# Kernel optimization log

Measured on AMD Instinct MI355X. Metric: run time of the kernel, lower is better.

The kernel has to match this reference:

```python
import jax, jax.numpy as jnp
import numpy as np
from jax import lax

B, Ht, Wt, C, NH, KV, FF = 32, 32, 32, 768, 12, 16, 4
HD = C // NH
EPS = 1e-5


def setup_inputs() -> dict:
    key = jax.random.key(0)
    ks = jax.random.split(key, 12)
    rn = lambda k, s, sc=0.02: jax.random.normal(k, s, jnp.float32) * sc
    inp = {"x": jax.random.normal(ks[0], (B, Ht * Wt, C), jnp.float32)}
    inp["ln1_g"] = jnp.ones((C,), jnp.float32)
    inp["ln1_b"] = jnp.zeros((C,), jnp.float32)
    for i, nm in enumerate(["q", "k", "v"]):
        inp[f"dw_w_{nm}"] = rn(ks[1 + i], (C, 1, 3, 3), 0.1)
        inp[f"dw_b_{nm}"] = jnp.zeros((C,), jnp.float32)
        inp[f"bn_g_{nm}"] = jnp.ones((C,), jnp.float32)
        inp[f"bn_b_{nm}"] = jnp.zeros((C,), jnp.float32)
        inp[f"bn_m_{nm}"] = jnp.zeros((C,), jnp.float32)
        inp[f"bn_v_{nm}"] = jnp.ones((C,), jnp.float32)
        inp[f"W_{nm}"] = rn(ks[4 + i], (C, C))
        inp[f"b_{nm}"] = jnp.zeros((C,), jnp.float32)
    inp["ln2_g"] = jnp.ones((C,), jnp.float32)
    inp["ln2_b"] = jnp.zeros((C,), jnp.float32)
    inp["W1"] = rn(ks[7], (FF * C, C))
    inp["b1"] = jnp.zeros((FF * C,), jnp.float32)
    inp["W2"] = rn(ks[8], (C, FF * C))
    inp["b2"] = jnp.zeros((C,), jnp.float32)
    return inp


def _ln(x, g, b):
    m = jnp.mean(x, -1, keepdims=True)
    v = jnp.var(x, -1, keepdims=True)
    return (x - m) * lax.rsqrt(v + EPS) * g + b


def _dw_branch(x4, w, bias, g, bb, m, v, stride):
    # depthwise conv (groups=C) -> ELU -> BatchNorm (eval) -> b (h w) c
    y = lax.conv_general_dilated(
        x4, w, (stride, stride), [(1, 1), (1, 1)],
        feature_group_count=C,
        dimension_numbers=("NCHW", "OIHW", "NCHW"),
    ) + bias[None, :, None, None]
    y = jax.nn.elu(y)
    y = (y - m[None, :, None, None]) * lax.rsqrt(v + EPS)[None, :, None, None] \
        * g[None, :, None, None] + bb[None, :, None, None]
    return y.reshape(B, C, -1).transpose(0, 2, 1)  # (B, n, C)


def _heads(t, Wm, bm):
    t = t @ Wm.T + bm                         # (B, n, C)
    n = t.shape[1]
    return t.reshape(B, n, NH, HD).transpose(0, 2, 1, 3)  # (B, H, n, d)


def reference(x, ln1_g, ln1_b,
              dw_w_q, dw_b_q, bn_g_q, bn_b_q, bn_m_q, bn_v_q, W_q, b_q,
              dw_w_k, dw_b_k, bn_g_k, bn_b_k, bn_m_k, bn_v_k, W_k, b_k,
              dw_w_v, dw_b_v, bn_g_v, bn_b_v, bn_m_v, bn_v_v, W_v, b_v,
              ln2_g, ln2_b, W1, b1, W2, b2):
    xn = _ln(x, ln1_g, ln1_b)
    x4 = xn.transpose(0, 2, 1).reshape(B, C, Ht, Wt)
    q = _heads(_dw_branch(x4, dw_w_q, dw_b_q, bn_g_q, bn_b_q, bn_m_q, bn_v_q, 1), W_q, b_q)
    k = _heads(_dw_branch(x4, dw_w_k, dw_b_k, bn_g_k, bn_b_k, bn_m_k, bn_v_k, 2), W_k, b_k)
    v = _heads(_dw_branch(x4, dw_w_v, dw_b_v, bn_g_v, bn_b_v, bn_m_v, bn_v_v, 2), W_v, b_v)
    scale = 1.0 / (HD ** 0.5)
    attn = jnp.einsum("bhnd,bhmd->bhnm", q, k) * scale
    attn = jax.nn.softmax(attn, axis=-1)
    o = jnp.einsum("bhnm,bhmd->bhnd", attn, v)
    o = o.transpose(0, 2, 1, 3).reshape(B, Ht * Wt, C)
    x = x + o  # DropPath is identity at inference
    h = _ln(x, ln2_g, ln2_b)
    h = jax.nn.gelu(h @ W1.T + b1, approximate=False) @ W2.T + b2
    return x + h
```

## Files before the change

### kernel.cpp

```cpp
#include <hip/hip_runtime.h>
#include <math.h>

#define NB   32
#define C_   768
#define NQ   1024
#define NKV  256
#define NH_  12
#define HD_  64
#define FFC  3072
#define EPS_ 1e-5f

typedef __attribute__((ext_vector_type(8))) _Float16 f16x8;
typedef __attribute__((ext_vector_type(4))) _Float16 f16x4;
typedef __attribute__((ext_vector_type(4))) float    f32x4;

__device__ __forceinline__ void gload_lds16(const void* g, void* l) {
  __builtin_amdgcn_global_load_lds((const __attribute__((address_space(1))) void*)g,
                                   (__attribute__((address_space(3))) void*)l, 16, 0, 0);
}

__global__ __launch_bounds__(256)
void ln_fwd_kernel(const float* __restrict__ x, const float* __restrict__ g,
                   const float* __restrict__ b, _Float16* __restrict__ out) {
  const int row = blockIdx.x;
  const float* xr = x + (size_t)row * C_;
  const int t = threadIdx.x;
  float v0 = xr[t], v1 = xr[t + 256], v2 = xr[t + 512];
  float s = v0 + v1 + v2;
  float q = v0 * v0 + v1 * v1 + v2 * v2;
#pragma unroll
  for (int m = 1; m < 64; m <<= 1) { s += __shfl_xor(s, m); q += __shfl_xor(q, m); }
  __shared__ float ls[4], lq[4];
  const int w = t >> 6, lane = t & 63;
  if (lane == 0) { ls[w] = s; lq[w] = q; }
  __syncthreads();
  s = ls[0] + ls[1] + ls[2] + ls[3];
  q = lq[0] + lq[1] + lq[2] + lq[3];
  const float mean = s * (1.f / C_);
  const float rstd = rsqrtf(q * (1.f / C_) - mean * mean + EPS_);
  _Float16* orow = out + (size_t)row * C_;
  orow[t]       = (_Float16)((v0 - mean) * rstd * g[t]       + b[t]);
  orow[t + 256] = (_Float16)((v1 - mean) * rstd * g[t + 256] + b[t + 256]);
  orow[t + 512] = (_Float16)((v2 - mean) * rstd * g[t + 512] + b[t + 512]);
}

__global__ __launch_bounds__(256)
void resln2_kernel(const float* __restrict__ x, const _Float16* __restrict__ o,
                   const float* __restrict__ g, const float* __restrict__ bb,
                   float* __restrict__ xr_out, _Float16* __restrict__ h) {
  const int row = blockIdx.x;
  const float* xp = x + (size_t)row * C_;
  const _Float16* op = o + (size_t)row * C_;
  const int t = threadIdx.x;
  float v[3]; float s = 0.f, q = 0.f;
#pragma unroll
  for (int i = 0; i < 3; i++) {
    int c = t + i * 256;
    v[i] = xp[c] + (float)op[c];
    s += v[i]; q += v[i] * v[i];
  }
#pragma unroll
  for (int m = 1; m < 64; m <<= 1) { s += __shfl_xor(s, m); q += __shfl_xor(q, m); }
  __shared__ float ls[4], lq[4];
  const int w = t >> 6, lane = t & 63;
  if (lane == 0) { ls[w] = s; lq[w] = q; }
  __syncthreads();
  s = ls[0] + ls[1] + ls[2] + ls[3];
  q = lq[0] + lq[1] + lq[2] + lq[3];
  const float mean = s * (1.f / C_);
  const float rstd = rsqrtf(q * (1.f / C_) - mean * mean + EPS_);
#pragma unroll
  for (int i = 0; i < 3; i++) {
    int c = t + i * 256;
    xr_out[(size_t)row * C_ + c] = v[i];
    h[(size_t)row * C_ + c] = (_Float16)((v[i] - mean) * rstd * g[c] + bb[c]);
  }
}

#define SZ_CC (C_ * C_)
#define SZ_CF (FFC * C_)
__global__ void cast_all_kernel(const float* __restrict__ Wq, const float* __restrict__ Wk,
                                const float* __restrict__ Wv, const float* __restrict__ W1,
                                const float* __restrict__ W2,
                                _Float16* __restrict__ oq, _Float16* __restrict__ ok,
                                _Float16* __restrict__ ov, _Float16* __restrict__ o1,
                                _Float16* __restrict__ o2) {
  const int total = 3 * SZ_CC + 2 * SZ_CF;
  int i = blockIdx.x * 256 + threadIdx.x;
  int stride = gridDim.x * 256;
  for (; i < total; i += stride) {
    if (i < SZ_CC)                     oq[i] = (_Float16)Wq[i];
    else if (i < 2 * SZ_CC)            ok[i - SZ_CC] = (_Float16)Wk[i - SZ_CC];
    else if (i < 3 * SZ_CC)            ov[i - 2 * SZ_CC] = (_Float16)Wv[i - 2 * SZ_CC];
    else if (i < 3 * SZ_CC + SZ_CF)    o1[i - 3 * SZ_CC] = (_Float16)W1[i - 3 * SZ_CC];
    else                               o2[i - 3 * SZ_CC - SZ_CF] = (_Float16)W2[i - 3 * SZ_CC - SZ_CF];
  }
}

__global__ __launch_bounds__(256)
void vtrans_kernel(const _Float16* __restrict__ vbuf, _Float16* __restrict__ vT) {
  const int b = blockIdx.z;
  const int c = blockIdx.y * 256 + threadIdx.x;
  const int kvb = blockIdx.x * 64;
#pragma unroll
  for (int kk = 0; kk < 8; kk++) {
    int kv0 = kvb + kk * 8;
    f16x8 v;
#pragma unroll
    for (int j = 0; j < 8; j++)
      v[j] = vbuf[(size_t)((b << 8) + kv0 + j) * C_ + c];
    *(f16x8*)(vT + ((size_t)(b * C_ + c) << 8) + kv0) = v;
  }
}

struct DwP { const float *w, *bias, *g, *b, *m, *v; };

__device__ __forceinline__ float elu_f(float x) {
  return x > 0.f ? x : __expf(x) - 1.f;
}

__global__ __launch_bounds__(256)
void dw_fused_kernel(const _Float16* __restrict__ xn, DwP pq, DwP pk, DwP pv,
                     _Float16* __restrict__ oq, _Float16* __restrict__ ok,
                     _Float16* __restrict__ ov) {
  const int i = blockIdx.x;
  const int b = blockIdx.z;
  const int c = blockIdx.y * 256 + threadIdx.x;
  const _Float16* xb = xn + (size_t)b * NQ * C_ + c;

  float wq[9], wk[9], wv[9];
#pragma unroll
  for (int u = 0; u < 9; u++) {
    wq[u] = pq.w[c * 9 + u]; wk[u] = pk.w[c * 9 + u]; wv[u] = pv.w[c * 9 + u];
  }
  const float skq = rsqrtf(pq.v[c] + EPS_) * pq.g[c], bnq = pq.b[c] - pq.m[c] * skq;
  const float skk = rsqrtf(pk.v[c] + EPS_) * pk.g[c], bnk = pk.b[c] - pk.m[c] * skk;
  const float skv = rsqrtf(pv.v[c] + EPS_) * pv.g[c], bnv = pv.b[c] - pv.m[c] * skv;
  const float cbq = pq.bias[c], cbk = pk.bias[c], cbv = pv.bias[c];

  float t[5][5];
  auto ldc = [&](int s, int iw) {
    const bool cv = (iw >= 0 && iw < 32);
#pragma unroll
    for (int u = 0; u < 5; u++) {
      int ih = 2 * i - 1 + u;
      t[u][s] = (cv && ih >= 0 && ih < 32) ? (float)xb[(size_t)(ih * 32 + iw) * C_] : 0.f;
    }
  };

#pragma unroll
  for (int j = 0; j < 16; j++) {
    if (j == 0) {
      ldc(0, -1); ldc(1, 0); ldc(2, 1); ldc(3, 2); ldc(4, 3);
    } else {
#pragma unroll
      for (int u = 0; u < 5; u++) { t[u][0] = t[u][2]; t[u][1] = t[u][3]; t[u][2] = t[u][4]; }
      ldc(3, 2 * j + 2); ldc(4, 2 * j + 3);
    }
    float ak = cbk, av = cbv;
#pragma unroll
    for (int u = 0; u < 3; u++)
#pragma unroll
      for (int vv = 0; vv < 3; vv++) {
        ak += t[u][vv] * wk[u * 3 + vv];
        av += t[u][vv] * wv[u * 3 + vv];
      }
    ak = elu_f(ak) * skk + bnk;
    av = elu_f(av) * skv + bnv;
    ok[((size_t)b * NKV + i * 16 + j) * C_ + c] = (_Float16)ak;
    ov[((size_t)b * NKV + i * 16 + j) * C_ + c] = (_Float16)av;
#pragma unroll
    for (int a = 0; a < 2; a++)
#pragma unroll
      for (int b2 = 0; b2 < 2; b2++) {
        float aq = cbq;
#pragma unroll
        for (int u = 0; u < 3; u++)
#pragma unroll
          for (int vv = 0; vv < 3; vv++)
            aq += t[a + u][b2 + vv] * wq[u * 3 + vv];
        aq = elu_f(aq) * skq + bnq;
        oq[((size_t)b * NQ + (2 * i + a) * 32 + (2 * j + b2)) * C_ + c] = (_Float16)aq;
      }
  }
}

__device__ __forceinline__ void stage_tile(const _Float16* __restrict__ src, int ldk,
                                           int row0, int kt, _Float16* lds, int w, int lane) {
#pragma unroll
  for (int it = 0; it < 4; it++) {
    int cid = (it * 4 + w) * 64 + lane;
    int row = cid >> 3, kg = cid & 7;
    int kgs = kg ^ (row & 7);
    const _Float16* g = src + (size_t)(row0 + row) * ldk + kt * 64 + kgs * 8;
    gload_lds16((const void*)g, (void*)((char*)lds + (it * 4 + w) * 1024));
  }
}

template <int EPI>
__global__ __launch_bounds__(256, 2)
void gemm_f16(const _Float16* __restrict__ A, const _Float16* __restrict__ Bw,
              const float* __restrict__ bias,
              _Float16* __restrict__ outh, float* __restrict__ outf,
              int M, int N, int K) {
  __shared__ __align__(16) _Float16 lds[2][2][128 * 64];
  const int tid = threadIdx.x, w = tid >> 6, lane = tid & 63;
  const int wm = w >> 1, wn = w & 1;
  const int m0 = blockIdx.x * 128, n0 = blockIdx.y * 128;

  f32x4 acc[4][4];
#pragma unroll
  for (int i = 0; i < 4; i++)
#pragma unroll
    for (int j = 0; j < 4; j++)
#pragma unroll
      for (int r = 0; r < 4; r++) acc[i][j][r] = 0.f;

  stage_tile(A, K, m0, 0, lds[0][0], w, lane);
  stage_tile(Bw, K, n0, 0, lds[0][1], w, lane);
  __syncthreads();
  const int NKT = K >> 6;
  int buf = 0;
  for (int kt = 0; kt < NKT; kt++) {
    if (kt + 1 < NKT) {
      stage_tile(A, K, m0, kt + 1, lds[buf ^ 1][0], w, lane);
      stage_tile(Bw, K, n0, kt + 1, lds[buf ^ 1][1], w, lane);
    }
    f16x8 af[4][2], bfr[4][2];
#pragma unroll
    for (int mi = 0; mi < 4; mi++)
#pragma unroll
      for (int kh = 0; kh < 2; kh++) {
        int row = wm * 64 + mi * 16 + (lane & 15);
        int kg = kh * 4 + (lane >> 4);
        af[mi][kh] = *(const f16x8*)&lds[buf][0][row * 64 + ((kg ^ (row & 7)) << 3)];
      }
#pragma unroll
    for (int ni = 0; ni < 4; ni++)
#pragma unroll
      for (int kh = 0; kh < 2; kh++) {
        int row = wn * 64 + ni * 16 + (lane & 15);
        int kg = kh * 4 + (lane >> 4);
        bfr[ni][kh] = *(const f16x8*)&lds[buf][1][row * 64 + ((kg ^ (row & 7)) << 3)];
      }
#pragma unroll
    for (int mi = 0; mi < 4; mi++)
#pragma unroll
      for (int ni = 0; ni < 4; ni++)
#pragma unroll
        for (int kh = 0; kh < 2; kh++)
          acc[mi][ni] = __builtin_amdgcn_mfma_f32_16x16x32_f16(af[mi][kh], bfr[ni][kh],
                                                               acc[mi][ni], 0, 0, 0);
    __syncthreads();
    buf ^= 1;
  }
#pragma unroll
  for (int mi = 0; mi < 4; mi++)
#pragma unroll
    for (int ni = 0; ni < 4; ni++) {
      int col = n0 + wn * 64 + ni * 16 + (lane & 15);
      float bv = bias[col];
#pragma unroll
      for (int r = 0; r < 4; r++) {
        int rowg = m0 + wm * 64 + mi * 16 + (lane >> 4) * 4 + r;
        float val = acc[mi][ni][r] + bv;
        size_t idx = (size_t)rowg * N + col;
        if (EPI == 0) {
          outh[idx] = (_Float16)val;
        } else if (EPI == 1) {
          float ge = 0.5f * val * (1.f + erff(val * 0.70710678118f));
          outh[idx] = (_Float16)ge;
        } else {
          outf[idx] += val;
        }
      }
    }
}

__global__ __launch_bounds__(512, 2)
void attn_kernel(const _Float16* __restrict__ Q, const _Float16* __restrict__ Kb,
                 const _Float16* __restrict__ vT, _Float16* __restrict__ O) {
  __shared__ __align__(16) _Float16 Klds[256 * 64];
  __shared__ __align__(16) _Float16 Vt[64 * 256];
  const int tid = threadIdx.x, w = tid >> 6, lane = tid & 63;
  const int hi = lane >> 4, lo = lane & 15;
  const int half = blockIdx.x & 1;
  const int h = (blockIdx.x >> 1) % NH_;
  const int b = blockIdx.x / (2 * NH_);

  const _Float16* qp = Q + (size_t)b * NQ * C_ + h * HD_;
  const _Float16* kp = Kb + (size_t)b * NKV * C_ + h * HD_;
  const _Float16* vp = vT + ((size_t)(b * C_ + h * HD_) << 8);

#pragma unroll
  for (int i = 0; i < 4; i++) {
    int cid = i * 512 + w * 64 + lane;
    int row = cid >> 3, kg = cid & 7;
    const _Float16* g = kp + (size_t)row * C_ + ((kg ^ (row & 7)) << 3);
    gload_lds16((const void*)g, (void*)((char*)Klds + (i * 512 + w * 64) * 16));
  }
#pragma unroll
  for (int i = 0; i < 4; i++) {
    int cid = i * 512 + w * 64 + lane;
    int row = cid >> 5, kg = cid & 31;
    const _Float16* g = vp + ((size_t)row << 8) + ((kg ^ (row & 7)) << 3);
    gload_lds16((const void*)g, (void*)((char*)Vt + (i * 512 + w * 64) * 16));
  }
  __syncthreads();

#pragma unroll
  for (int ti = 0; ti < 4; ti++) {
    const int q0 = half * 512 + w * 64 + ti * 16;
    f16x8 qf[2];
#pragma unroll
    for (int kh = 0; kh < 2; kh++)
      qf[kh] = *(const f16x8*)(qp + (size_t)(q0 + lo) * C_ + kh * 32 + hi * 8);
    f32x4 S[16];
#pragma unroll
    for (int nt = 0; nt < 16; nt++) {
      f32x4 s; s[0] = 0.f; s[1] = 0.f; s[2] = 0.f; s[3] = 0.f;
      const _Float16* krow = &Klds[(nt * 16 + lo) * 64];
#pragma unroll
      for (int kh = 0; kh < 2; kh++) {
        f16x8 kf = *(const f16x8*)&krow[((kh * 4 + hi) ^ (lo & 7)) << 3];
        s = __builtin_amdgcn_mfma_f32_16x16x32_f16(kf, qf[kh], s, 0, 0, 0);
      }
      S[nt] = s;
    }
    float mx = -1e30f;
#pragma unroll
    for (int nt = 0; nt < 16; nt++)
#pragma unroll
      for (int r = 0; r < 4; r++) { S[nt][r] *= 0.125f; mx = fmaxf(mx, S[nt][r]); }
    mx = fmaxf(mx, __shfl_xor(mx, 16));
    mx = fmaxf(mx, __shfl_xor(mx, 32));
    float sum = 0.f;
#pragma unroll
    for (int nt = 0; nt < 16; nt++)
#pragma unroll
      for (int r = 0; r < 4; r++) { float e = __expf(S[nt][r] - mx); S[nt][r] = e; sum += e; }
    sum += __shfl_xor(sum, 16);
    sum += __shfl_xor(sum, 32);
    const float inv = 1.f / sum;
    f16x8 pa8[8];
#pragma unroll
    for (int ntp = 0; ntp < 8; ntp++)
#pragma unroll
      for (int r = 0; r < 4; r++) {
        pa8[ntp][r]     = (_Float16)(S[2 * ntp][r] * inv);
        pa8[ntp][4 + r] = (_Float16)(S[2 * ntp + 1][r] * inv);
      }
    f32x4 acc[4];
#pragma unroll
    for (int dt = 0; dt < 4; dt++) { acc[dt][0] = 0.f; acc[dt][1] = 0.f; acc[dt][2] = 0.f; acc[dt][3] = 0.f; }
#pragma unroll
    for (int dt = 0; dt < 4; dt++) {
      const int d = dt * 16 + lo, sw = d & 7;
      const _Float16* vrow = &Vt[d * 256 + 4 * (hi & 1)];
#pragma unroll
      for (int ntp = 0; ntp < 8; ntp++) {
        f16x4 v0 = *(const f16x4*)&vrow[((4 * ntp + (hi >> 1)) ^ sw) << 3];
        f16x4 v1 = *(const f16x4*)&vrow[((4 * ntp + 2 + (hi >> 1)) ^ sw) << 3];
        f16x8 vt8;
#pragma unroll
        for (int r = 0; r < 4; r++) { vt8[r] = v0[r]; vt8[4 + r] = v1[r]; }
        acc[dt] = __builtin_amdgcn_mfma_f32_16x16x32_f16(pa8[ntp], vt8, acc[dt], 0, 0, 0);
      }
    }
#pragma unroll
    for (int dt = 0; dt < 4; dt++)
#pragma unroll
      for (int r = 0; r < 4; r++)
        O[(size_t)(b * NQ + q0 + 4 * hi + r) * C_ + h * HD_ + dt * 16 + lo] = (_Float16)acc[dt][r];
  }
}

extern "C" void kernel_launch(void* const* d_in, const int* in_sizes, int n_in,
                              void* d_out, int out_size, void* d_ws, size_t ws_size,
                              hipStream_t stream) {
  (void)in_sizes; (void)n_in; (void)out_size; (void)ws_size;
  const float* x    = (const float*)d_in[0];
  const float* ln1g = (const float*)d_in[1];
  const float* ln1b = (const float*)d_in[2];
  DwP pq { (const float*)d_in[3], (const float*)d_in[4], (const float*)d_in[5],
           (const float*)d_in[6], (const float*)d_in[7], (const float*)d_in[8] };
  const float* Wq = (const float*)d_in[9];  const float* bq = (const float*)d_in[10];
  DwP pk { (const float*)d_in[11], (const float*)d_in[12], (const float*)d_in[13],
           (const float*)d_in[14], (const float*)d_in[15], (const float*)d_in[16] };
  const float* Wk = (const float*)d_in[17]; const float* bk = (const float*)d_in[18];
  DwP pv { (const float*)d_in[19], (const float*)d_in[20], (const float*)d_in[21],
           (const float*)d_in[22], (const float*)d_in[23], (const float*)d_in[24] };
  const float* Wv = (const float*)d_in[25]; const float* bv = (const float*)d_in[26];
  const float* ln2g = (const float*)d_in[27];
  const float* ln2b = (const float*)d_in[28];
  const float* W1 = (const float*)d_in[29]; const float* b1 = (const float*)d_in[30];
  const float* W2 = (const float*)d_in[31]; const float* b2 = (const float*)d_in[32];

  char* ws = (char*)d_ws;
  _Float16* xn   = (_Float16*)(ws + 0);
  _Float16* o    = xn;
  _Float16* tq   = (_Float16*)(ws + 100663296);
  _Float16* tk   = (_Float16*)(ws + 150994944);
  _Float16* tv   = (_Float16*)(ws + 163577856);
  _Float16* hb   = tq;
  _Float16* vTb  = tv;
  _Float16* qb   = (_Float16*)(ws + 176160768);
  _Float16* gbuf = qb;
  _Float16* kb   = (_Float16*)(ws + 226492416);
  _Float16* vbuf = (_Float16*)(ws + 239075328);
  _Float16* wqh  = (_Float16*)(ws + 251658240);
  _Float16* wkh  = (_Float16*)(ws + 252837888);
  _Float16* wvh  = (_Float16*)(ws + 254017536);
  _Float16* w1h  = (_Float16*)(ws + 255197184);
  _Float16* w2h  = (_Float16*)(ws + 259915776);
  float* out = (float*)d_out;

  ln_fwd_kernel<<<NB * NQ, 256, 0, stream>>>(x, ln1g, ln1b, xn);
  cast_all_kernel<<<2048, 256, 0, stream>>>(Wq, Wk, Wv, W1, W2, wqh, wkh, wvh, w1h, w2h);
  dw_fused_kernel<<<dim3(16, 3, NB), 256, 0, stream>>>(xn, pq, pk, pv, tq, tk, tv);
  gemm_f16<0><<<dim3(256, 6), 256, 0, stream>>>(tq, wqh, bq, qb, nullptr, NB * NQ, C_, C_);
  gemm_f16<0><<<dim3(64, 6), 256, 0, stream>>>(tk, wkh, bk, kb, nullptr, NB * NKV, C_, C_);
  gemm_f16<0><<<dim3(64, 6), 256, 0, stream>>>(tv, wvh, bv, vbuf, nullptr, NB * NKV, C_, C_);
  vtrans_kernel<<<dim3(4, 3, NB), 256, 0, stream>>>(vbuf, vTb);
  attn_kernel<<<NB * NH_ * 2, 512, 0, stream>>>(qb, kb, vTb, o);
  resln2_kernel<<<NB * NQ, 256, 0, stream>>>(x, o, ln2g, ln2b, out, hb);
  for (int mc = 0; mc < 4; mc++) {
    gemm_f16<1><<<dim3(64, 24), 256, 0, stream>>>(hb + (size_t)mc * 8192 * C_, w1h, b1,
                                                  gbuf, nullptr, 8192, FFC, C_);
    gemm_f16<2><<<dim3(64, 6), 256, 0, stream>>>(gbuf, w2h, b2, nullptr,
                                                 out + (size_t)mc * 8192 * C_, 8192, C_, FFC);
  }
}
```

Baseline: 930.6 us.

## Add 256x256-tile GELU GEMM for FFN1, vectorize depthwise conv over channel pairs

Adds a new 512-thread GEMM kernel with 256x256 tiles and a GELU epilogue for the first FFN projection. It uses s_setprio around the MFMA bursts and splits each k-tile into four phases. The FFN now runs in two M-chunks of 16384 rows instead of four chunks of 8192, with the GELU buffer moved to the start of the workspace. The depthwise conv kernel now has each thread handle two adjacent channels with f16x2 loads and stores, using a single 384-thread block per row across all 768 channels. The aim is more data reuse per LDS load in the dominant FFN GEMM and fewer memory transactions in the conv. The cost is higher register and LDS pressure (128 KB LDS per block), which may reduce occupancy.

```diff
diff --git a/kernel.cpp b/kernel.cpp
--- a/kernel.cpp
+++ b/kernel.cpp
@@ -12,6 +12,7 @@
 
 typedef __attribute__((ext_vector_type(8))) _Float16 f16x8;
 typedef __attribute__((ext_vector_type(4))) _Float16 f16x4;
+typedef __attribute__((ext_vector_type(2))) _Float16 f16x2;
 typedef __attribute__((ext_vector_type(4))) float    f32x4;
 
 __device__ __forceinline__ void gload_lds16(const void* g, void* l) {
@@ -119,32 +120,42 @@
   return x > 0.f ? x : __expf(x) - 1.f;
 }
 
-__global__ __launch_bounds__(256)
+__global__ __launch_bounds__(384)
 void dw_fused_kernel(const _Float16* __restrict__ xn, DwP pq, DwP pk, DwP pv,
                      _Float16* __restrict__ oq, _Float16* __restrict__ ok,
                      _Float16* __restrict__ ov) {
   const int i = blockIdx.x;
   const int b = blockIdx.z;
-  const int c = blockIdx.y * 256 + threadIdx.x;
-  const _Float16* xb = xn + (size_t)b * NQ * C_ + c;
-
-  float wq[9], wk[9], wv[9];
+  const int c0 = 2 * threadIdx.x;
+  const _Float16* xb = xn + (size_t)b * NQ * C_ + c0;
+
+  float wqx[9], wqy[9], wkx[9], wky[9], wvx[9], wvy[9];
 #pragma unroll
   for (int u = 0; u < 9; u++) {
-    wq[u] = pq.w[c * 9 + u]; wk[u] = pk.w[c * 9 + u]; wv[u] = pv.w[c * 9 + u];
-  }
-  const float skq = rsqrtf(pq.v[c] + EPS_) * pq.g[c], bnq = pq.b[c] - pq.m[c] * skq;
-  const float skk = rsqrtf(pk.v[c] + EPS_) * pk.g[c], bnk = pk.b[c] - pk.m[c] * skk;
-  const float skv = rsqrtf(pv.v[c] + EPS_) * pv.g[c], bnv = pv.b[c] - pv.m[c] * skv;
-  const float cbq = pq.bias[c], cbk = pk.bias[c], cbv = pv.bias[c];
-
-  float t[5][5];
+    wqx[u] = pq.w[c0 * 9 + u]; wqy[u] = pq.w[(c0 + 1) * 9 + u];
+    wkx[u] = pk.w[c0 * 9 + u]; wky[u] = pk.w[(c0 + 1) * 9 + u];
+    wvx[u] = pv.w[c0 * 9 + u]; wvy[u] = pv.w[(c0 + 1) * 9 + u];
+  }
+  const float skqx = rsqrtf(pq.v[c0] + EPS_) * pq.g[c0], bnqx = pq.b[c0] - pq.m[c0] * skqx;
+  const float skqy = rsqrtf(pq.v[c0+1] + EPS_) * pq.g[c0+1], bnqy = pq.b[c0+1] - pq.m[c0+1] * skqy;
+  const float skkx = rsqrtf(pk.v[c0] + EPS_) * pk.g[c0], bnkx = pk.b[c0] - pk.m[c0] * skkx;
+  const float skky = rsqrtf(pk.v[c0+1] + EPS_) * pk.g[c0+1], bnky = pk.b[c0+1] - pk.m[c0+1] * skky;
+  const float skvx = rsqrtf(pv.v[c0] + EPS_) * pv.g[c0], bnvx = pv.b[c0] - pv.m[c0] * skvx;
+  const float skvy = rsqrtf(pv.v[c0+1] + EPS_) * pv.g[c0+1], bnvy = pv.b[c0+1] - pv.m[c0+1] * skvy;
+  const float cbqx = pq.bias[c0], cbqy = pq.bias[c0+1];
+  const float cbkx = pk.bias[c0], cbky = pk.bias[c0+1];
+  const float cbvx = pv.bias[c0], cbvy = pv.bias[c0+1];
+
+  float tx[5][5], ty[5][5];
   auto ldc = [&](int s, int iw) {
     const bool cv = (iw >= 0 && iw < 32);
 #pragma unroll
     for (int u = 0; u < 5; u++) {
       int ih = 2 * i - 1 + u;
-      t[u][s] = (cv && ih >= 0 && ih < 32) ? (float)xb[(size_t)(ih * 32 + iw) * C_] : 0.f;
+      if (cv && ih >= 0 && ih < 32) {
+        f16x2 p = *(const f16x2*)&xb[(size_t)(ih * 32 + iw) * C_];
+        tx[u][s] = (float)p[0]; ty[u][s] = (float)p[1];
+      } else { tx[u][s] = 0.f; ty[u][s] = 0.f; }
     }
   };
 
@@ -154,33 +165,43 @@
       ldc(0, -1); ldc(1, 0); ldc(2, 1); ldc(3, 2); ldc(4, 3);
     } else {
 #pragma unroll
-      for (int u = 0; u < 5; u++) { t[u][0] = t[u][2]; t[u][1] = t[u][3]; t[u][2] = t[u][4]; }
+      for (int u = 0; u < 5; u++) {
+        tx[u][0] = tx[u][2]; tx[u][1] = tx[u][3]; tx[u][2] = tx[u][4];
+        ty[u][0] = ty[u][2]; ty[u][1] = ty[u][3]; ty[u][2] = ty[u][4];
+      }
       ldc(3, 2 * j + 2); ldc(4, 2 * j + 3);
     }
-    float ak = cbk, av = cbv;
+    float akx = cbkx, aky = cbky, avx = cbvx, avy = cbvy;
 #pragma unroll
     for (int u = 0; u < 3; u++)
 #pragma unroll
       for (int vv = 0; vv < 3; vv++) {
-        ak += t[u][vv] * wk[u * 3 + vv];
-        av += t[u][vv] * wv[u * 3 + vv];
-      }
-    ak = elu_f(ak) * skk + bnk;
-    av = elu_f(av) * skv + bnv;
-    ok[((size_t)b * NKV + i * 16 + j) * C_ + c] = (_Float16)ak;
-    ov[((size_t)b * NKV + i * 16 + j) * C_ + c] = (_Float16)av;
+        akx += tx[u][vv] * wkx[u * 3 + vv]; aky += ty[u][vv] * wky[u * 3 + vv];
+        avx += tx[u][vv] * wvx[u * 3 + vv]; avy += ty[u][vv] * wvy[u * 3 + vv];
+      }
+    f16x2 kv2, vv2;
+    kv2[0] = (_Float16)(elu_f(akx) * skkx + bnkx);
+    kv2[1] = (_Float16)(elu_f(aky) * skky + bnky);
+    vv2[0] = (_Float16)(elu_f(avx) * skvx + bnvx);
+    vv2[1] = (_Float16)(elu_f(avy) * skvy + bnvy);
+    *(f16x2*)&ok[((size_t)b * NKV + i * 16 + j) * C_ + c0] = kv2;
+    *(f16x2*)&ov[((size_t)b * NKV + i * 16 + j) * C_ + c0] = vv2;
 #pragma unroll
     for (int a = 0; a < 2; a++)
 #pragma unroll
       for (int b2 = 0; b2 < 2; b2++) {
-        float aq = cbq;
+        float aqx = cbqx, aqy = cbqy;
 #pragma unroll
         for (int u = 0; u < 3; u++)
 #pragma unroll
-          for (int vv = 0; vv < 3; vv++)
-            aq += t[a + u][b2 + vv] * wq[u * 3 + vv];
-        aq = elu_f(aq) * skq + bnq;
-        oq[((size_t)b * NQ + (2 * i + a) * 32 + (2 * j + b2)) * C_ + c] = (_Float16)aq;
+          for (int vv = 0; vv < 3; vv++) {
+            aqx += tx[a + u][b2 + vv] * wqx[u * 3 + vv];
+            aqy += ty[a + u][b2 + vv] * wqy[u * 3 + vv];
+          }
+        f16x2 q2;
+        q2[0] = (_Float16)(elu_f(aqx) * skqx + bnqx);
+        q2[1] = (_Float16)(elu_f(aqy) * skqy + bnqy);
+        *(f16x2*)&oq[((size_t)b * NQ + (2 * i + a) * 32 + (2 * j + b2)) * C_ + c0] = q2;
       }
   }
 }
@@ -265,14 +286,98 @@
         int rowg = m0 + wm * 64 + mi * 16 + (lane >> 4) * 4 + r;
         float val = acc[mi][ni][r] + bv;
         size_t idx = (size_t)rowg * N + col;
-        if (EPI == 0) {
-          outh[idx] = (_Float16)val;
-        } else if (EPI == 1) {
-          float ge = 0.5f * val * (1.f + erff(val * 0.70710678118f));
-          outh[idx] = (_Float16)ge;
-        } else {
-          outf[idx] += val;
+        if (EPI == 0) outh[idx] = (_Float16)val;
+        else          outf[idx] += val;
+      }
+    }
+}
+
+__global__ __launch_bounds__(512, 2)
+void gemm256_gelu(const _Float16* __restrict__ A, const _Float16* __restrict__ Bw,
+                  const float* __restrict__ bias, _Float16* __restrict__ outh,
+                  int M, int N, int K) {
+  __shared__ __align__(16) _Float16 As[2][256 * 64];
+  __shared__ __align__(16) _Float16 Bs[2][256 * 64];
+  const int tid = threadIdx.x, w = tid >> 6, lane = tid & 63;
+  const int wm = w >> 2, wn = w & 3;
+  const int hi = lane >> 4, lo = lane & 15;
+  const int m0 = blockIdx.x * 256, n0 = blockIdx.y * 256;
+
+  f32x4 acc[8][4];
+#pragma unroll
+  for (int i = 0; i < 8; i++)
+#pragma unroll
+    for (int j = 0; j < 4; j++)
+#pragma unroll
+      for (int r = 0; r < 4; r++) acc[i][j][r] = 0.f;
+
+  auto stage = [&](const _Float16* src, int row0, int kt, _Float16* lds) {
+#pragma unroll
+    for (int it = 0; it < 4; it++) {
+      int cid = it * 512 + tid;
+      int row = cid >> 3, kg = cid & 7;
+      const _Float16* g = src + (size_t)(row0 + row) * K + kt * 64 + ((kg ^ (row & 7)) << 3);
+      gload_lds16((const void*)g, (void*)((char*)lds + (size_t)(it * 512 + w * 64) * 16));
+    }
+  };
+
+  stage(A, m0, 0, As[0]);
+  stage(Bw, n0, 0, Bs[0]);
+  __syncthreads();
+  const int NKT = K >> 6;
+  int buf = 0;
+  for (int kt = 0; kt < NKT; kt++) {
+    if (kt + 1 < NKT) {
+      stage(A, m0, kt + 1, As[buf ^ 1]);
+      stage(Bw, n0, kt + 1, Bs[buf ^ 1]);
+    }
+#pragma unroll
+    for (int ph = 0; ph < 4; ph++) {
+      const int mh = ph & 1, nh = ph >> 1;
+      f16x8 af[4][2], bf[2][2];
+#pragma unroll
+      for (int mi = 0; mi < 4; mi++)
+#pragma unroll
+        for (int kh = 0; kh < 2; kh++) {
+          int row = wm * 128 + mh * 64 + mi * 16 + lo;
+          int kg = kh * 4 + hi;
+          af[mi][kh] = *(const f16x8*)&As[buf][row * 64 + ((kg ^ (row & 7)) << 3)];
         }
+#pragma unroll
+      for (int ni = 0; ni < 2; ni++)
+#pragma unroll
+        for (int kh = 0; kh < 2; kh++) {
+          int row = wn * 64 + nh * 32 + ni * 16 + lo;
+          int kg = kh * 4 + hi;
+          bf[ni][kh] = *(const f16x8*)&Bs[buf][row * 64 + ((kg ^ (row & 7)) << 3)];
+        }
+      __builtin_amdgcn_s_setprio(1);
+#pragma unroll
+      for (int mi = 0; mi < 4; mi++)
+#pragma unroll
+        for (int ni = 0; ni < 2; ni++)
+#pragma unroll
+          for (int kh = 0; kh < 2; kh++)
+            acc[mh * 4 + mi][nh * 2 + ni] =
+                __builtin_amdgcn_mfma_f32_16x16x32_f16(af[mi][kh], bf[ni][kh],
+                                                       acc[mh * 4 + mi][nh * 2 + ni], 0, 0, 0);
+      __builtin_amdgcn_s_setprio(0);
+    }
+    __syncthreads();
+    buf ^= 1;
+  }
+#pragma unroll
+  for (int mq = 0; mq < 8; mq++)
+#pragma unroll
+    for (int nf = 0; nf < 4; nf++) {
+      int col = n0 + wn * 64 + nf * 16 + lo;
+      float bv = bias[col];
+#pragma unroll
+      for (int r = 0; r < 4; r++) {
+        int rowg = m0 + wm * 128 + mq * 16 + hi * 4 + r;
+        float val = acc[mq][nf][r] + bv;
+        float ge = 0.5f * val * (1.f + erff(val * 0.70710678118f));
+        outh[(size_t)rowg * N + col] = (_Float16)ge;
       }
     }
 }
@@ -399,13 +504,13 @@
   char* ws = (char*)d_ws;
   _Float16* xn   = (_Float16*)(ws + 0);
   _Float16* o    = xn;
+  _Float16* gbuf = (_Float16*)(ws + 0);
   _Float16* tq   = (_Float16*)(ws + 100663296);
   _Float16* tk   = (_Float16*)(ws + 150994944);
   _Float16* tv   = (_Float16*)(ws + 163577856);
   _Float16* hb   = tq;
   _Float16* vTb  = tv;
   _Float16* qb   = (_Float16*)(ws + 176160768);
-  _Float16* gbuf = qb;
   _Float16* kb   = (_Float16*)(ws + 226492416);
   _Float16* vbuf = (_Float16*)(ws + 239075328);
   _Float16* wqh  = (_Float16*)(ws + 251658240);
@@ -417,17 +522,17 @@
 
   ln_fwd_kernel<<<NB * NQ, 256, 0, stream>>>(x, ln1g, ln1b, xn);
   cast_all_kernel<<<2048, 256, 0, stream>>>(Wq, Wk, Wv, W1, W2, wqh, wkh, wvh, w1h, w2h);
-  dw_fused_kernel<<<dim3(16, 3, NB), 256, 0, stream>>>(xn, pq, pk, pv, tq, tk, tv);
+  dw_fused_kernel<<<dim3(16, 1, NB), 384, 0, stream>>>(xn, pq, pk, pv, tq, tk, tv);
   gemm_f16<0><<<dim3(256, 6), 256, 0, stream>>>(tq, wqh, bq, qb, nullptr, NB * NQ, C_, C_);
   gemm_f16<0><<<dim3(64, 6), 256, 0, stream>>>(tk, wkh, bk, kb, nullptr, NB * NKV, C_, C_);
   gemm_f16<0><<<dim3(64, 6), 256, 0, stream>>>(tv, wvh, bv, vbuf, nullptr, NB * NKV, C_, C_);
   vtrans_kernel<<<dim3(4, 3, NB), 256, 0, stream>>>(vbuf, vTb);
   attn_kernel<<<NB * NH_ * 2, 512, 0, stream>>>(qb, kb, vTb, o);
   resln2_kernel<<<NB * NQ, 256, 0, stream>>>(x, o, ln2g, ln2b, out, hb);
-  for (int mc = 0; mc < 4; mc++) {
-    gemm_f16<1><<<dim3(64, 24), 256, 0, stream>>>(hb + (size_t)mc * 8192 * C_, w1h, b1,
-                                                  gbuf, nullptr, 8192, FFC, C_);
-    gemm_f16<2><<<dim3(64, 6), 256, 0, stream>>>(gbuf, w2h, b2, nullptr,
-                                                 out + (size_t)mc * 8192 * C_, 8192, C_, FFC);
-  }
-}
+  for (int mc = 0; mc < 2; mc++) {
+    gemm256_gelu<<<dim3(64, 12), 512, 0, stream>>>(hb + (size_t)mc * 16384 * C_, w1h, b1,
+                                                   gbuf, 16384, FFC, C_);
+    gemm_f16<2><<<dim3(128, 6), 256, 0, stream>>>(gbuf, w2h, b2, nullptr,
+                                                  out + (size_t)mc * 16384 * C_, 16384, C_, FFC);
+  }
+}
```

New measurement: 908.6 us. -2.4%, faster.
